# Kernel optimization log

Measured on AMD Instinct MI355X. Metric: run time of the kernel, lower is better.

The kernel has to match this reference:

```python
import jax, jax.numpy as jnp
import numpy as np

LMBDA = 100.0
GAMMA = 0.5  # resolvant_gamma


def setup_inputs() -> dict:
    key = jax.random.key(0)
    ks = jax.random.split(key, 8)
    B, Vx, Vy, C, K = 1, 5000, 5000, 128, 64
    feat_x = jax.random.normal(ks[0], (B, Vx, C), dtype=jnp.float32)
    feat_y = jax.random.normal(ks[1], (B, Vy, C), dtype=jnp.float32)
    # positive, sorted eigenvalues (Laplacian spectrum)
    evals_x = jnp.sort(jax.random.uniform(ks[2], (B, K), minval=0.01, maxval=10.0), axis=-1)
    evals_y = jnp.sort(jax.random.uniform(ks[3], (B, K), minval=0.01, maxval=10.0), axis=-1)
    # pseudo-inverse eigenvector rows, scaled ~1/sqrt(V) for realistic magnitudes
    evecs_trans_x = jax.random.normal(ks[4], (B, K, Vx), dtype=jnp.float32) / np.sqrt(Vx)
    evecs_trans_y = jax.random.normal(ks[5], (B, K, Vy), dtype=jnp.float32) / np.sqrt(Vy)
    # sqrt mass matrices: well-conditioned near-identity (must be invertible)
    eye = jnp.eye(K, dtype=jnp.float32)
    sqrtMk_x = eye[None] + 0.05 * jax.random.normal(ks[6], (B, K, K), dtype=jnp.float32)
    sqrtMk_y = eye[None] + 0.05 * jax.random.normal(ks[7], (B, K, K), dtype=jnp.float32)
    return {
        "feat_x": feat_x, "feat_y": feat_y,
        "evals_x": evals_x, "evals_y": evals_y,
        "evecs_trans_x": evecs_trans_x, "evecs_trans_y": evecs_trans_y,
        "sqrtMk_x": sqrtMk_x, "sqrtMk_y": sqrtMk_y,
    }


def _compute_fmap(fx, fy, ex, ey, Px, Py, Mx, My):
    # fx:[V,C] fy:[V,C] ex,ey:[K] Px,Py:[K,V] Mx,My:[K,K]
    A = Px @ fx                 # [K,C] spectral coeffs of source feats
    Bc = My @ (Py @ fy)         # adapt_feature=True: [K,C]
    k, m = A.shape
    vec_B = Bc.T.reshape(m * k, 1)
    # Ik = sqrtMk_y (adapt_feature, no dev_feature)
    At_Ik = jnp.kron(A.T, My)   # [m*k, k*k]
    first = At_Ik.T @ At_Ik     # [k*k, k*k]
    # adapt_mask=True branch: resolvent mask as Kronecker operators
    inv_Mx = jnp.linalg.inv(Mx)
    s = jnp.maximum(jnp.max(ex), jnp.max(ey))
    g1 = (ex / s) ** GAMMA
    g2 = (ey / s) ** GAMMA
    rn1_re = g1 / (g1 * g1 + 1.0)
    rn1_im = 1.0 / (g1 * g1 + 1.0)
    rn2_re = g2 / (g2 * g2 + 1.0)
    rn2_im = 1.0 / (g2 * g2 + 1.0)
    lx_re = jnp.kron(rn1_re[:, None] * inv_Mx, My)          # diag(rn1_re)@inv_Mx
    lx_im = jnp.kron(rn1_im[:, None] * inv_Mx, My)
    ly_re = jnp.kron(inv_Mx, My * rn2_re[None, :])          # My@diag(rn2_re)
    ly_im = jnp.kron(inv_Mx, My * rn2_im[None, :])
    D_re = ly_re - lx_re
    D_im = ly_im - lx_im
    second = D_re.T @ D_re + D_im.T @ D_im
    rhs = At_Ik.T @ vec_B
    op = first + LMBDA * second
    C = jnp.linalg.solve(op, rhs).reshape(k, k).T
    return C[None]  # [1,K,K]


def reference(feat_x, feat_y, evals_x, evals_y, evecs_trans_x, evecs_trans_y, sqrtMk_x, sqrtMk_y):
    Cxy = _compute_fmap(
        feat_x[0], feat_y[0], evals_x[0], evals_y[0],
        evecs_trans_x[0], evecs_trans_y[0], sqrtMk_x[0], sqrtMk_y[0],
    )
    return Cxy  # bidirectional=False -> Cyx is None
```

## Files before the change

kernel.cpp:

```cpp
#include <hip/hip_runtime.h>

#define NV 5000
#define LMB 100.0f
#define MAXIT 150
#define TOL 1e-10f
#define NBLK 32
#define NALL 96
#define BSZ 512

#define SV_O     0
#define CTRL_O   256
#define PART_O   2048
#define AH_O     657408
#define B0_O     665600
#define H_O      673792
#define E_O      677888
#define Z2_O     681984
#define ZH_O     686080
#define Q0_O     690176
#define LIH_O    702464
#define LIE_O    706560
#define U0_O     710656
#define LH_O     747520
#define BT_O     751616
#define RSTK_O   755712
#define LCT_O    772096
#define WG_O     788480
#define XG_O     792576
#define WS_NEED  796672

#define MS_O     PART_O
#define PRT2_O   (PART_O + 16384)
#define ZERO_N   35712

#define LCTS_S   0
#define RPK_S    12288
#define TPART_S  12800
#define TPACK_S  15920
#define SPART_S  16304
#define SM_FLOATS 21504

typedef unsigned long long u64;
union PKu { u64 u; float2 f; };

__device__ __forceinline__ float aload(const float* p) {
  return __hip_atomic_load(p, __ATOMIC_RELAXED, __HIP_MEMORY_SCOPE_AGENT);
}
__device__ __forceinline__ void astore(float* p, float v) {
  __hip_atomic_store(p, v, __ATOMIC_RELAXED, __HIP_MEMORY_SCOPE_AGENT);
}
__device__ __forceinline__ u64 aload64(const u64* p) {
  return __hip_atomic_load(p, __ATOMIC_RELAXED, __HIP_MEMORY_SCOPE_AGENT);
}
__device__ __forceinline__ void astore64(u64* p, u64 v) {
  __hip_atomic_store(p, v, __ATOMIC_RELAXED, __HIP_MEMORY_SCOPE_AGENT);
}

__device__ __forceinline__ void gbar(int* cnt, int target) {
  __syncthreads();
  if (threadIdx.x == 0) {
    __hip_atomic_fetch_add(cnt, 1, __ATOMIC_ACQ_REL, __HIP_MEMORY_SCOPE_AGENT);
    while (__hip_atomic_load(cnt, __ATOMIC_ACQUIRE, __HIP_MEMORY_SCOPE_AGENT) < target) {
      __builtin_amdgcn_s_sleep(2);
    }
  }
  __syncthreads();
}

__device__ __forceinline__ void stageN(float* dst, const float* src) {
  for (int e = threadIdx.x; e < 4096; e += BSZ)
    dst[(e >> 6) * 65 + (e & 63)] = src[e];
}
__device__ __forceinline__ void stageT(float* dst, const float* src) {
  for (int e = threadIdx.x; e < 4096; e += BSZ)
    dst[(e & 63) * 65 + (e >> 6)] = src[e];
}
__device__ __forceinline__ void mm65(const float* Ls, const float* Rs, float* D) {
  for (int e = threadIdx.x; e < 4096; e += BSZ) {
    int i = e >> 6, j = e & 63;
    float a0 = 0.f, a1 = 0.f;
#pragma unroll 8
    for (int t = 0; t < 64; t += 2) {
      a0 = fmaf(Ls[i * 65 + t], Rs[t * 65 + j], a0);
      a1 = fmaf(Ls[i * 65 + t + 1], Rs[(t + 1) * 65 + j], a1);
    }
    D[e] = a0 + a1;
  }
}
__device__ __forceinline__ void mm65L(const float* Ls, const float* Rs, float* DL) {
  for (int e = threadIdx.x; e < 4096; e += BSZ) {
    int i = e >> 6, j = e & 63;
    float a0 = 0.f, a1 = 0.f;
#pragma unroll 8
    for (int t = 0; t < 64; t += 2) {
      a0 = fmaf(Ls[i * 65 + t], Rs[t * 65 + j], a0);
      a1 = fmaf(Ls[i * 65 + t + 1], Rs[(t + 1) * 65 + j], a1);
    }
    DL[i * 65 + j] = a0 + a1;
  }
}
__device__ void mmNN_s(const float* L, const float* R, float* D, float* sm) {
  stageN(sm, L); stageN(sm + 4160, R);
  __syncthreads();
  mm65(sm, sm + 4160, D);
}

__device__ void chol_inv(const float* S, float* Li, float* Lf, float* sm) {
  float (*M)[65] = (float (*)[65])sm;
  float (*T)[65] = (float (*)[65])(sm + 64 * 65);
  int tid = threadIdx.x;
  for (int e = tid; e < 4096; e += BSZ) {
    M[e >> 6][e & 63] = S[e];
    T[e >> 6][e & 63] = 0.f;
  }
  __syncthreads();
  for (int j = 0; j < 64; ++j) {
    float pv = M[j][j];
    __syncthreads();
    float sc = rsqrtf(pv);
    if (tid < 64 - j) M[j + tid][j] *= sc;
    __syncthreads();
    int m = 63 - j, c2 = (m * (m + 1)) >> 1;
    for (int e = tid; e < c2; e += BSZ) {
      int rp = (int)((sqrtf(8.f * (float)e + 1.f) - 1.f) * 0.5f);
      while (((rp + 1) * (rp + 2)) >> 1 <= e) ++rp;
      while ((rp * (rp + 1)) >> 1 > e) --rp;
      int cp = e - ((rp * (rp + 1)) >> 1);
      int r = j + 1 + rp, c = j + 1 + cp;
      M[r][c] = fmaf(-M[r][j], M[c][j], M[r][c]);
    }
    __syncthreads();
  }
  if (tid < 64) {
    int c = tid;
    T[c][c] = 1.f / M[c][c];
    for (int r = c + 1; r < 64; ++r) {
      float s = 0.f;
      for (int t = c; t < r; ++t) s = fmaf(M[r][t], T[t][c], s);
      T[r][c] = -s / M[r][r];
    }
  }
  __syncthreads();
  if (Lf) {
    for (int e = tid; e < 4096; e += BSZ) {
      int r = e >> 6, c = e & 63;
      Lf[e] = (r >= c) ? M[r][c] : 0.f;
    }
  }
  for (int e = tid; e < 4096; e += BSZ) Li[e] = T[e >> 6][e & 63];
}

__device__ __forceinline__ float coop_apply(float* sm, const float* yv, float y_own,
                                            int lane, int wv8) {
  const float* LCTs = sm + LCTS_S;
  const float* Rpk = sm + RPK_S;
  float* Tpart = sm + TPART_S;
  float* Tpack = sm + TPACK_S;
  float* Spart = sm + SPART_S;
  float t1p[6];
#pragma unroll
  for (int p = 0; p < 6; ++p) t1p[p] = 0.f;
#pragma unroll
  for (int u = 0; u < 8; ++u) {
    int m = u * 8 + wv8;
    float yu = yv[u];
    float4 rA = *(const float4*)&Rpk[m * 8 + 0];
    float2 rB = *(const float2*)&Rpk[m * 8 + 4];
    t1p[0] = fmaf(yu, rA.x, t1p[0]);  t1p[1] = fmaf(yu, rA.y, t1p[1]);
    t1p[2] = fmaf(yu, rA.z, t1p[2]);  t1p[3] = fmaf(yu, rA.w, t1p[3]);
    t1p[4] = fmaf(yu, rB.x, t1p[4]);  t1p[5] = fmaf(yu, rB.y, t1p[5]);
  }
#pragma unroll
  for (int p = 0; p < 6; ++p) Tpart[wv8 * 390 + p * 65 + lane] = t1p[p];
  __syncthreads();
  int tid = wv8 * 64 + lane;
  if (tid < 384) {
    int tk = tid >> 1, c = tid & 1;
    int p = (tk >> 6) * 2 + c, k = tk & 63;
    Tpack[tid] = (((Tpart[0 * 390 + p * 65 + k] + Tpart[1 * 390 + p * 65 + k]) +
                   (Tpart[2 * 390 + p * 65 + k] + Tpart[3 * 390 + p * 65 + k])) +
                  ((Tpart[4 * 390 + p * 65 + k] + Tpart[5 * 390 + p * 65 + k]) +
                   (Tpart[6 * 390 + p * 65 + k] + Tpart[7 * 390 + p * 65 + k])));
  }
  __syncthreads();
  float s0 = 0.f, s1 = 0.f;
  int tk0 = wv8 * 24;
#pragma unroll 8
  for (int q = 0; q < 24; ++q) {
    int tk = tk0 + q;
    float lv = LCTs[tk * 64 + lane];
    float2 tv = *(const float2*)&Tpack[tk * 2];
    s0 = fmaf(lv, tv.x, s0);
    s1 = fmaf(lv, tv.y, s1);
  }
  Spart[wv8 * 128 + 0 * 64 + lane] = s0;
  Spart[wv8 * 128 + 1 * 64 + lane] = s1;
  __syncthreads();
  int cw = (wv8 & 1) * 64 + lane;
  return y_own + (((Spart[0 * 128 + cw] + Spart[1 * 128 + cw]) +
                   (Spart[2 * 128 + cw] + Spart[3 * 128 + cw])) +
                  ((Spart[4 * 128 + cw] + Spart[5 * 128 + cw]) +
                   (Spart[6 * 128 + cw] + Spart[7 * 128 + cw])));
}

__global__ __launch_bounds__(BSZ) void solve_kernel(const float* fx, const float* fy,
                                                    const float* ex, const float* ey,
                                                    const float* Px, const float* Py,
                                                    const float* Mx, const float* My,
                                                    float* W, float* out) {
  __shared__ float sm[SM_FLOATS] __attribute__((aligned(16)));
  __shared__ float sLd[192], sRd[192], wred[4], scal[2];
  int tid = threadIdx.x, blk = blockIdx.x;
  int* cnt = (int*)(W + CTRL_O);

  if (blk < 80) {
    int mat = (blk >= 40), seg = mat ? (blk - 40) : blk;
    const float* P = (mat ? Py : Px);
    const float* f = (mat ? fy : fx);
    int v0 = seg * 125;
    for (int e = tid; e < 8000; e += BSZ) {
      int rr = e / 125, vv = e - rr * 125;
      sm[rr * 126 + vv] = P[rr * NV + v0 + vv];
    }
    __syncthreads();
    int rg = (tid >> 5) << 2;
    int cq = (tid & 31) << 2;
    float acc[4][4];
#pragma unroll
    for (int u = 0; u < 4; ++u)
#pragma unroll
      for (int v = 0; v < 4; ++v) acc[u][v] = 0.f;
    for (int v5 = 0; v5 < 125; v5 += 5) {
      float4 fv[5];
#pragma unroll
      for (int q = 0; q < 5; ++q)
        fv[q] = *(const float4*)(f + (size_t)(v0 + v5 + q) * 128 + cq);
#pragma unroll
      for (int q = 0; q < 5; ++q) {
#pragma unroll
        for (int u = 0; u < 4; ++u) {
          float pv = sm[(rg + u) * 126 + v5 + q];
          acc[u][0] = fmaf(pv, fv[q].x, acc[u][0]);
          acc[u][1] = fmaf(pv, fv[q].y, acc[u][1]);
          acc[u][2] = fmaf(pv, fv[q].z, acc[u][2]);
          acc[u][3] = fmaf(pv, fv[q].w, acc[u][3]);
        }
      }
    }
    float* O = W + PART_O + (size_t)blk * 8192;
#pragma unroll
    for (int u = 0; u < 4; ++u) {
      float4 o = make_float4(acc[u][0], acc[u][1], acc[u][2], acc[u][3]);
      *(float4*)(O + (rg + u) * 128 + cq) = o;
    }
  } else if (blk < 82) {
    for (int e = tid; e < 4096; e += BSZ) sm[(e >> 6) * 65 + (e & 63)] = My[e];
    __syncthreads();
    int base = (blk - 80) * 2048;
    for (int e = tid; e < 2048; e += BSZ) {
      int i = (base + e) >> 6, j = (base + e) & 63;
      float a0 = 0.f, a1 = 0.f;
#pragma unroll 8
      for (int t = 0; t < 64; t += 2) {
        a0 = fmaf(sm[t * 65 + i], sm[t * 65 + j], a0);
        a1 = fmaf(sm[(t + 1) * 65 + i], sm[(t + 1) * 65 + j], a1);
      }
      W[H_O + base + e] = a0 + a1;
    }
  } else if (blk == 82) {
    if (tid < 64) {
      float vx = ex[tid], vy = ey[tid];
      float m = fmaxf(vx, vy);
#pragma unroll
      for (int o = 32; o > 0; o >>= 1) m = fmaxf(m, __shfl_xor(m, o, 64));
      float g1 = sqrtf(vx / m), g2 = sqrtf(vy / m);
      float d1 = 1.f / fmaf(g1, g1, 1.f), d2 = 1.f / fmaf(g2, g2, 1.f);
      W[SV_O + tid] = g1 * d1;
      W[SV_O + 64 + tid] = d1;
      W[SV_O + 128 + tid] = g2 * d2;
      W[SV_O + 192 + tid] = d2;
    }
  }
  gbar(cnt, NALL);
  if (blk >= NBLK) return;

  if (blk == 0) {
    chol_inv(W + H_O, W + LIH_O, W + LH_O, sm);
  } else if (blk <= 19) {
    int item = blk;
    if (item <= 8) {
      int c0 = (item - 1) * 16;
      float* ssum = sm;
      float* mxs = sm + 1088;
      for (int e = tid; e < 4096; e += BSZ) mxs[(e >> 6) * 65 + (e & 63)] = Mx[e];
      for (int e = tid; e < 1024; e += BSZ) {
        int t = e >> 4, cl = e & 15;
        float s = 0.f;
        for (int p = 0; p < 40; ++p) s += W[PART_O + (size_t)p * 8192 + t * 128 + c0 + cl];
        ssum[t * 17 + cl] = s;
      }
      __syncthreads();
      for (int e = tid; e < 1024; e += BSZ) {
        int i = e >> 4, cl = e & 15;
        float a0 = 0.f, a1 = 0.f;
#pragma unroll 8
        for (int t = 0; t < 64; t += 2) {
          a0 = fmaf(mxs[t * 65 + i], ssum[t * 17 + cl], a0);
          a1 = fmaf(mxs[(t + 1) * 65 + i], ssum[(t + 1) * 17 + cl], a1);
        }
        W[AH_O + i * 128 + c0 + cl] = a0 + a1;
      }
    } else if (item <= 16) {
      int base = (item - 9) * 1024;
      for (int e = tid; e < 1024; e += BSZ) {
        float s = 0.f;
        for (int p = 0; p < 40; ++p) s += W[PART_O + (size_t)(40 + p) * 8192 + base + e];
        W[B0_O + base + e] = s;
      }
    } else {
      if (tid < 256) sm[tid] = W[SV_O + tid];
      __syncthreads();
      int t = item - 17;
      for (int e = tid; e < 4096; e += BSZ) {
        int k = e >> 6, b = e & 63;
        float h = W[H_O + e], v;
        if (t == 0) v = h * (sm[128 + k] * sm[128 + b] + sm[192 + k] * sm[192 + b]);
        else if (t == 1) v = h * (sm[128 + k] + sm[128 + b]);
        else v = h * (sm[192 + k] + sm[192 + b]);
        W[Q0_O + t * 4096 + e] = v;
      }
    }
  }
  gbar(cnt, NALL + NBLK);

  if (blk < 4) {
    for (int e = tid; e < 8192; e += BSZ) {
      int i = e >> 7, c = e & 127;
      sm[c * 65 + i] = W[AH_O + e];
    }
    __syncthreads();
    int i0 = blk * 16;
    for (int e = tid; e < 1024; e += BSZ) {
      int i = i0 + (e >> 6), j = e & 63;
      float a0 = 0.f, a1 = 0.f;
#pragma unroll 8
      for (int c = 0; c < 128; c += 2) {
        a0 = fmaf(sm[c * 65 + i], sm[c * 65 + j], a0);
        a1 = fmaf(sm[(c + 1) * 65 + i], sm[(c + 1) * 65 + j], a1);
      }
      float acc = a0 + a1;
      if (i == j) {
        float a = W[SV_O + i], b = W[SV_O + 64 + i];
        acc += LMB * (a * a + b * b);
      }
      W[E_O + i * 64 + j] = acc;
    }
  } else if (blk < 8) {
    int i0 = (blk - 4) * 16;
    for (int e = tid; e < 8192; e += BSZ) {
      int j = e >> 7, c = e & 127;
      sm[c * 65 + j] = W[B0_O + e];
    }
    for (int e = tid; e < 2048; e += BSZ) {
      int il = e >> 7, c = e & 127;
      sm[8320 + c * 17 + il] = W[AH_O + (i0 + il) * 128 + c];
    }
    __syncthreads();
    for (int e = tid; e < 1024; e += BSZ) {
      int il = e >> 6, j = e & 63;
      float a0 = 0.f, a1 = 0.f;
#pragma unroll 8
      for (int c = 0; c < 128; c += 2) {
        a0 = fmaf(sm[8320 + c * 17 + il], sm[c * 65 + j], a0);
        a1 = fmaf(sm[8320 + (c + 1) * 17 + il], sm[(c + 1) * 65 + j], a1);
      }
      W[Z2_O + (i0 + il) * 64 + j] = a0 + a1;
    }
  } else if (blk < 11) {
    int t = blk - 8;
    mmNN_s(W + LIH_O, W + Q0_O + t * 4096, W + U0_O + t * 4096, sm);
  } else {
    for (int e = (blk - 11) * BSZ + tid; e < ZERO_N; e += 21 * BSZ)
      W[MS_O + e] = 0.f;
  }
  gbar(cnt, NALL + 2 * NBLK);

  if (blk == 0) chol_inv(W + E_O, W + LIE_O, nullptr, sm);
  else if (blk == 1) mmNN_s(W + Z2_O, W + LH_O, W + ZH_O, sm);
  else if (blk < 5) {
    int t = blk - 2;
    stageN(sm, W + U0_O + t * 4096);
    stageT(sm + 4160, W + LIH_O);
    __syncthreads();
    mm65L(sm, sm + 4160, sm + 8320);
    __syncthreads();
    for (int e = tid; e < 4096; e += BSZ) {
      int a = e >> 6, b = e & 63;
      W[RSTK_O + t * 4096 + e] = 0.5f * (sm[8320 + a * 65 + b] + sm[8320 + b * 65 + a]);
    }
  }
  gbar(cnt, NALL + 3 * NBLK);

  if (blk == 0) mmNN_s(W + LIE_O, W + ZH_O, W + BT_O, sm);
  else if (blk == 1) {
    stageN(sm, W + LIE_O);
    stageT(sm + 4160, W + LIE_O);
    __syncthreads();
    mm65L(sm, sm + 4160, sm + 8320);
    __syncthreads();
    for (int e = tid; e < 4096; e += BSZ) {
      int k = e >> 6, i = e & 63;
      W[LCT_O + e] = LMB * 0.5f * (sm[8320 + k * 65 + i] + sm[8320 + i * 65 + k]);
    }
  } else if (blk < 4) {
    float* dv = sLd;
    if (tid < 64) dv[tid] = W[SV_O + ((blk == 2) ? tid : 64 + tid)];
    stageN(sm, W + LIE_O);
    __syncthreads();
    for (int e = tid; e < 4096; e += BSZ) {
      int jq = e >> 6, k = e & 63;
      sm[4160 + k * 65 + jq] = sm[jq * 65 + k] * dv[k];
    }
    __syncthreads();
    mm65L(sm, sm + 4160, sm + 8320);
    __syncthreads();
    int t = blk - 1;
    for (int e = tid; e < 4096; e += BSZ) {
      int k = e >> 6, i = e & 63;
      W[LCT_O + t * 4096 + e] = -LMB * 0.5f * (sm[8320 + k * 65 + i] + sm[8320 + i * 65 + k]);
    }
  }
  gbar(cnt, NALL + 4 * NBLK);

  int lane = tid & 63, wv8 = tid >> 6;
  int jown = blk * 2 + wv8;
  const float* BTp = W + BT_O;
  const float* LCTp = W + LCT_O;
  const float* RSTKp = W + RSTK_O;
  u64* MS = (u64*)(W + MS_O);
  u64* PR2 = (u64*)(W + PRT2_O);

  for (int e = tid; e < 12288; e += BSZ) sm[LCTS_S + e] = LCTp[e];
  if (tid < 384) {
    int m = tid / 6, p = tid - m * 6;
    int t = p >> 1, c = p & 1;
    sm[RPK_S + m * 8 + p] = RSTKp[(t * 64 + blk * 2 + c) * 64 + m];
  }
  if (tid < 192) {
    int t = tid >> 6, i = tid & 63;
    sLd[tid] = LCTp[t * 4096 + i * 64 + i];
    sRd[tid] = RSTKp[t * 4096 + i * 64 + i];
  }
  __syncthreads();
  float yv0[8];
#pragma unroll
  for (int u = 0; u < 8; ++u) {
    int col = u * 8 + wv8;
    float den = 1.f + sLd[lane] * sRd[col] + sLd[64 + lane] * sRd[64 + col] +
                sLd[128 + lane] * sRd[128 + col];
    yv0[u] = BTp[lane * 64 + col] / den;
  }
  float invd = 0.f, u_l = 0.f, r_l = 0.f, m_l = 0.f;
  if (wv8 < 2) {
    invd = 1.f / (1.f + sLd[lane] * sRd[jown] + sLd[64 + lane] * sRd[64 + jown] +
                  sLd[128 + lane] * sRd[128 + jown]);
    u_l = BTp[lane * 64 + jown] * invd;
    r_l = BTp[lane * 64 + jown];
  }
  float w_l = coop_apply(sm, yv0, u_l, lane, wv8);
  if (wv8 < 2) {
    m_l = invd * w_l;
    PKu pk; pk.f = make_float2(m_l, 1.f);
    astore64(MS + jown * 64 + lane, pk.u);
    float vr = r_l * u_l, vw = w_l * u_l;
#pragma unroll
    for (int o = 32; o; o >>= 1) { vr += __shfl_down(vr, o, 64); vw += __shfl_down(vw, o, 64); }
    if (lane == 0) { wred[wv8 * 2] = vr; wred[wv8 * 2 + 1] = vw; }
  }
  __syncthreads();
  if (tid == 0) {
    PKu a, b;
    a.f = make_float2(wred[0] + wred[2], 1.f);
    b.f = make_float2(wred[1] + wred[3], 1.f);
    astore64(PR2 + (size_t)blk * 2, a.u);
    astore64(PR2 + (size_t)blk * 2 + 1, b.u);
  }

  float p_l = 0.f, q_l = 0.f, z_l = 0.f, s_l = 0.f, x_l = 0.f;
  float gprev = 1.f, aprev = 1.f, g0b = 1.f;
  int sl = lane & 31;
  for (int j = 0; j < MAXIT; ++j) {
    unsigned sbits = __float_as_uint((float)(j + 1));
    const u64* msrc = MS + (size_t)(j & 1) * 4096;
    u64 raw[8];
#pragma unroll
    for (int u = 0; u < 8; ++u) raw[u] = aload64(msrc + u * BSZ + tid);
    const u64* ps = PR2 + ((size_t)j * 32 + sl) * 2;
    u64 ra = 0, rb = 0;
    if (wv8 == 0) { ra = aload64(ps); rb = aload64(ps + 1); }
    {
      int spins = 0;
      for (;;) {
        bool ok = true;
#pragma unroll
        for (int u = 0; u < 8; ++u) ok = ok && ((unsigned)(raw[u] >> 32) == sbits);
        if (__all(ok)) break;
        if (++spins > 64) {
          __hip_atomic_load(msrc + tid, __ATOMIC_ACQUIRE, __HIP_MEMORY_SCOPE_AGENT);
          spins = 0;
        }
#pragma unroll
        for (int u = 0; u < 8; ++u)
          if ((unsigned)(raw[u] >> 32) != sbits) raw[u] = aload64(msrc + u * BSZ + tid);
      }
    }
    float mv[8];
#pragma unroll
    for (int u = 0; u < 8; ++u) mv[u] = __uint_as_float((unsigned)raw[u]);
    float n_l = coop_apply(sm, mv, m_l, lane, wv8);
    if (wv8 == 0) {
      int spins = 0;
      for (;;) {
        bool ok = ((unsigned)(ra >> 32) == sbits) && ((unsigned)(rb >> 32) == sbits);
        if (__all(ok)) break;
        if (++spins > 64) {
          __hip_atomic_load(ps, __ATOMIC_ACQUIRE, __HIP_MEMORY_SCOPE_AGENT);
          spins = 0;
        }
        if ((unsigned)(ra >> 32) != sbits) ra = aload64(ps);
        if ((unsigned)(rb >> 32) != sbits) rb = aload64(ps + 1);
      }
      float pr = __uint_as_float((unsigned)ra), pw = __uint_as_float((unsigned)rb);
#pragma unroll
      for (int mm = 1; mm < 32; mm <<= 1) {
        pr += __shfl_xor(pr, mm, 64);
        pw += __shfl_xor(pw, mm, 64);
      }
      if (lane == 0) { scal[0] = pr; scal[1] = pw; }
    }
    __syncthreads();
    float gjb = scal[0], djb = scal[1];
    if (j == 0) g0b = gjb;
    if (j > 0 && fabsf(gjb) < TOL * fabsf(g0b)) break;
    if (wv8 < 2) {
      float bj = (j == 0) ? 0.f : gjb / gprev;
      float aj = (j == 0) ? gjb / djb : gjb / (djb - bj * gjb / aprev);
      float z_n = fmaf(bj, z_l, n_l);
      float w_n = fmaf(-aj, z_n, w_l);
      float m_n = invd * w_n;
      PKu pk; pk.f = make_float2(m_n, (float)(j + 2));
      astore64(MS + (size_t)((j + 1) & 1) * 4096 + jown * 64 + lane, pk.u);
      q_l = fmaf(bj, q_l, m_l);
      s_l = fmaf(bj, s_l, w_l);
      p_l = fmaf(bj, p_l, u_l);
      x_l = fmaf(aj, p_l, x_l);
      r_l = fmaf(-aj, s_l, r_l);
      u_l = fmaf(-aj, q_l, u_l);
      z_l = z_n; w_l = w_n; m_l = m_n;
      float vr = r_l * u_l, vw = w_l * u_l;
#pragma unroll
      for (int o = 32; o; o >>= 1) { vr += __shfl_down(vr, o, 64); vw += __shfl_down(vw, o, 64); }
      if (lane == 0) { wred[wv8 * 2] = vr; wred[wv8 * 2 + 1] = vw; }
      gprev = gjb; aprev = aj;
    }
    __syncthreads();
    if (tid == 0) {
      PKu a, b;
      a.f = make_float2(wred[0] + wred[2], (float)(j + 2));
      b.f = make_float2(wred[1] + wred[3], (float)(j + 2));
      astore64(PR2 + ((size_t)(j + 1) * 32 + blk) * 2, a.u);
      astore64(PR2 + ((size_t)(j + 1) * 32 + blk) * 2 + 1, b.u);
    }
  }
  if (wv8 < 2) astore(W + XG_O + jown * 64 + lane, x_l);
  gbar(cnt, NALL + 5 * NBLK);

  if (blk == 0) {
    float* Ys = sm;
    float* Ms2 = sm + 4160;
    for (int e = tid; e < 4096; e += BSZ) Ys[(e >> 6) * 65 + (e & 63)] = aload(W + XG_O + e);
    for (int e = tid; e < 4096; e += BSZ) Ms2[(e >> 6) * 65 + (e & 63)] = W[LIE_O + e];
    __syncthreads();
    for (int e = tid; e < 4096; e += BSZ) {
      int t = e >> 6, b = e & 63;
      float acc = 0.f;
#pragma unroll 8
      for (int a = 0; a < 64; ++a) acc = fmaf(Ms2[a * 65 + t], Ys[b * 65 + a], acc);
      W[WG_O + t * 64 + b] = acc;
    }
    __syncthreads();
    for (int e = tid; e < 4096; e += BSZ) Ys[(e >> 6) * 65 + (e & 63)] = W[WG_O + e];
    for (int e = tid; e < 4096; e += BSZ) Ms2[(e >> 6) * 65 + (e & 63)] = W[LIH_O + e];
    __syncthreads();
    for (int e = tid; e < 4096; e += BSZ) {
      int t = e >> 6, c = e & 63;
      float acc = 0.f;
#pragma unroll 8
      for (int b = 0; b < 64; ++b) acc = fmaf(Ys[t * 65 + b], Ms2[b * 65 + c], acc);
      W[WG_O + t * 64 + c] = acc;
    }
    __syncthreads();
    for (int e = tid; e < 4096; e += BSZ) Ys[(e >> 6) * 65 + (e & 63)] = W[WG_O + e];
    for (int e = tid; e < 4096; e += BSZ) Ms2[(e & 63) * 65 + (e >> 6)] = Mx[e];
    __syncthreads();
    for (int e = tid; e < 4096; e += BSZ) {
      int r = e >> 6, c = e & 63;
      float acc = 0.f;
#pragma unroll 8
      for (int t = 0; t < 64; ++t) acc = fmaf(Ms2[t * 65 + c], Ys[t * 65 + r], acc);
      out[e] = acc;
    }
  }
}

extern "C" void kernel_launch(void* const* d_in, const int* in_sizes, int n_in,
                              void* d_out, int out_size, void* d_ws, size_t ws_size,
                              hipStream_t stream) {
  const float* fx = (const float*)d_in[0];
  const float* fy = (const float*)d_in[1];
  const float* ex = (const float*)d_in[2];
  const float* ey = (const float*)d_in[3];
  const float* Px = (const float*)d_in[4];
  const float* Py = (const float*)d_in[5];
  const float* Mx = (const float*)d_in[6];
  const float* My = (const float*)d_in[7];
  float* out = (float*)d_out;
  float* W = (float*)d_ws;

  if (ws_size < (size_t)WS_NEED * sizeof(float)) {
    hipMemsetAsync(d_out, 0, (size_t)out_size * sizeof(float), stream);
    return;
  }

  hipMemsetAsync(W + CTRL_O, 0, 256, stream);
  solve_kernel<<<NALL, BSZ, 0, stream>>>(fx, fy, ex, ey, Px, Py, Mx, My, W, out);
}
```

Baseline: 342.4 us.

## Shard grid barrier counters and overlap dependency waits with partial matvec

```diff
diff --git a/kernel.cpp b/kernel.cpp
--- a/kernel.cpp
+++ b/kernel.cpp
@@ -56,11 +56,18 @@
   __hip_atomic_store(p, v, __ATOMIC_RELAXED, __HIP_MEMORY_SCOPE_AGENT);
 }
 
-__device__ __forceinline__ void gbar(int* cnt, int target) {
-  __syncthreads();
-  if (threadIdx.x == 0) {
-    __hip_atomic_fetch_add(cnt, 1, __ATOMIC_ACQ_REL, __HIP_MEMORY_SCOPE_AGENT);
-    while (__hip_atomic_load(cnt, __ATOMIC_ACQUIRE, __HIP_MEMORY_SCOPE_AGENT) < target) {
+__device__ __forceinline__ void gbar(int* cb, int phase, int blk, int per) {
+  __syncthreads();
+  if (threadIdx.x == 0)
+    __hip_atomic_fetch_add(cb + phase * 128 + (blk & 7) * 16, 1,
+                           __ATOMIC_ACQ_REL, __HIP_MEMORY_SCOPE_AGENT);
+  if (threadIdx.x < 64) {
+    for (;;) {
+      int v = (threadIdx.x < 8)
+        ? __hip_atomic_load(cb + phase * 128 + threadIdx.x * 16,
+                            __ATOMIC_ACQUIRE, __HIP_MEMORY_SCOPE_AGENT)
+        : per;
+      if (__all(v >= per)) break;
       __builtin_amdgcn_s_sleep(2);
     }
   }
@@ -115,10 +122,7 @@
   }
   __syncthreads();
   for (int j = 0; j < 64; ++j) {
-    float pv = M[j][j];
-    __syncthreads();
-    float sc = rsqrtf(pv);
-    if (tid < 64 - j) M[j + tid][j] *= sc;
+    if (tid < 63 - j) M[j + 1 + tid][j] *= rsqrtf(M[j][j]);
     __syncthreads();
     int m = 63 - j, c2 = (m * (m + 1)) >> 1;
     for (int e = tid; e < c2; e += BSZ) {
@@ -133,18 +137,18 @@
   }
   if (tid < 64) {
     int c = tid;
-    T[c][c] = 1.f / M[c][c];
+    T[c][c] = rsqrtf(M[c][c]);
     for (int r = c + 1; r < 64; ++r) {
       float s = 0.f;
       for (int t = c; t < r; ++t) s = fmaf(M[r][t], T[t][c], s);
-      T[r][c] = -s / M[r][r];
+      T[r][c] = -s * rsqrtf(M[r][r]);
     }
   }
   __syncthreads();
   if (Lf) {
     for (int e = tid; e < 4096; e += BSZ) {
       int r = e >> 6, c = e & 63;
-      Lf[e] = (r >= c) ? M[r][c] : 0.f;
+      Lf[e] = (r > c) ? M[r][c] : ((r == c) ? sqrtf(M[r][c]) : 0.f);
     }
   }
   for (int e = tid; e < 4096; e += BSZ) Li[e] = T[e >> 6][e & 63];
@@ -211,7 +215,7 @@
   __shared__ float sm[SM_FLOATS] __attribute__((aligned(16)));
   __shared__ float sLd[192], sRd[192], wred[4], scal[2];
   int tid = threadIdx.x, blk = blockIdx.x;
-  int* cnt = (int*)(W + CTRL_O);
+  int* cb = (int*)(W + CTRL_O);
 
   if (blk < 80) {
     int mat = (blk >= 40), seg = mat ? (blk - 40) : blk;
@@ -281,7 +285,7 @@
       W[SV_O + 192 + tid] = d2;
     }
   }
-  gbar(cnt, NALL);
+  gbar(cb, 0, blk, 12);
   if (blk >= NBLK) return;
 
   if (blk == 0) {
@@ -331,7 +335,7 @@
       }
     }
   }
-  gbar(cnt, NALL + NBLK);
+  gbar(cb, 1, blk, 4);
 
   if (blk < 4) {
     for (int e = tid; e < 8192; e += BSZ) {
@@ -383,7 +387,7 @@
     for (int e = (blk - 11) * BSZ + tid; e < ZERO_N; e += 21 * BSZ)
       W[MS_O + e] = 0.f;
   }
-  gbar(cnt, NALL + 2 * NBLK);
+  gbar(cb, 2, blk, 4);
 
   if (blk == 0) chol_inv(W + E_O, W + LIE_O, nullptr, sm);
   else if (blk == 1) mmNN_s(W + Z2_O, W + LH_O, W + ZH_O, sm);
@@ -399,7 +403,7 @@
       W[RSTK_O + t * 4096 + e] = 0.5f * (sm[8320 + a * 65 + b] + sm[8320 + b * 65 + a]);
     }
   }
-  gbar(cnt, NALL + 3 * NBLK);
+  gbar(cb, 3, blk, 4);
 
   if (blk == 0) mmNN_s(W + LIE_O, W + ZH_O, W + BT_O, sm);
   else if (blk == 1) {
@@ -430,7 +434,7 @@
       W[LCT_O + t * 4096 + e] = -LMB * 0.5f * (sm[8320 + k * 65 + i] + sm[8320 + i * 65 + k]);
     }
   }
-  gbar(cnt, NALL + 4 * NBLK);
+  gbar(cb, 4, blk, 4);
 
   int lane = tid & 63, wv8 = tid >> 6;
   int jown = blk * 2 + wv8;
@@ -439,6 +443,11 @@
   const float* RSTKp = W + RSTK_O;
   u64* MS = (u64*)(W + MS_O);
   u64* PR2 = (u64*)(W + PRT2_O);
+  const float* LCTs = sm + LCTS_S;
+  const float* Rpk = sm + RPK_S;
+  float* Tpart = sm + TPART_S;
+  float* Tpack = sm + TPACK_S;
+  float* Spart = sm + SPART_S;
 
   for (int e = tid; e < 12288; e += BSZ) sm[LCTS_S + e] = LCTp[e];
   if (tid < 384) {
@@ -492,40 +501,63 @@
   for (int j = 0; j < MAXIT; ++j) {
     unsigned sbits = __float_as_uint((float)(j + 1));
     const u64* msrc = MS + (size_t)(j & 1) * 4096;
-    u64 raw[8];
-#pragma unroll
-    for (int u = 0; u < 8; ++u) raw[u] = aload64(msrc + u * BSZ + tid);
     const u64* ps = PR2 + ((size_t)j * 32 + sl) * 2;
     u64 ra = 0, rb = 0;
     if (wv8 == 0) { ra = aload64(ps); rb = aload64(ps + 1); }
-    {
-      int spins = 0;
-      for (;;) {
-        bool ok = true;
-#pragma unroll
-        for (int u = 0; u < 8; ++u) ok = ok && ((unsigned)(raw[u] >> 32) == sbits);
-        if (__all(ok)) break;
-        if (++spins > 64) {
-          __hip_atomic_load(msrc + tid, __ATOMIC_ACQUIRE, __HIP_MEMORY_SCOPE_AGENT);
-          spins = 0;
+    float t1p[6];
+#pragma unroll
+    for (int p = 0; p < 6; ++p) t1p[p] = 0.f;
+    u64 raw8[8];
+#pragma unroll
+    for (int u = 0; u < 8; ++u) raw8[u] = aload64(msrc + u * BSZ + tid);
+    unsigned done = 0;
+    int spins = 0;
+    while (done != 0xFFu) {
+#pragma unroll
+      for (int u = 0; u < 8; ++u) {
+        if (!((done >> u) & 1u)) {
+          u64 v = raw8[u];
+          if ((unsigned)(v >> 32) == sbits) {
+            float yu = __uint_as_float((unsigned)v);
+            int m = u * 8 + wv8;
+            float4 rA = *(const float4*)&Rpk[m * 8 + 0];
+            float2 rB = *(const float2*)&Rpk[m * 8 + 4];
+            t1p[0] = fmaf(yu, rA.x, t1p[0]);
+            t1p[1] = fmaf(yu, rA.y, t1p[1]);
+            t1p[2] = fmaf(yu, rA.z, t1p[2]);
+            t1p[3] = fmaf(yu, rA.w, t1p[3]);
+            t1p[4] = fmaf(yu, rB.x, t1p[4]);
+            t1p[5] = fmaf(yu, rB.y, t1p[5]);
+            done |= (1u << u);
+          } else {
+            raw8[u] = aload64(msrc + u * BSZ + tid);
+          }
         }
-#pragma unroll
-        for (int u = 0; u < 8; ++u)
-          if ((unsigned)(raw[u] >> 32) != sbits) raw[u] = aload64(msrc + u * BSZ + tid);
-      }
-    }
-    float mv[8];
-#pragma unroll
-    for (int u = 0; u < 8; ++u) mv[u] = __uint_as_float((unsigned)raw[u]);
-    float n_l = coop_apply(sm, mv, m_l, lane, wv8);
-    if (wv8 == 0) {
-      int spins = 0;
+      }
+      if (done != 0xFFu && ++spins > 64) {
+        __hip_atomic_load(msrc + tid, __ATOMIC_ACQUIRE, __HIP_MEMORY_SCOPE_AGENT);
+        spins = 0;
+      }
+    }
+#pragma unroll
+    for (int p = 0; p < 6; ++p) Tpart[wv8 * 390 + p * 65 + lane] = t1p[p];
+    __syncthreads();
+    if (wv8 >= 2) {
+      int z = tid - 128;
+      int tk = z >> 1, c = z & 1;
+      int p = (tk >> 6) * 2 + c, k = tk & 63;
+      Tpack[z] = (((Tpart[0 * 390 + p * 65 + k] + Tpart[1 * 390 + p * 65 + k]) +
+                   (Tpart[2 * 390 + p * 65 + k] + Tpart[3 * 390 + p * 65 + k])) +
+                  ((Tpart[4 * 390 + p * 65 + k] + Tpart[5 * 390 + p * 65 + k]) +
+                   (Tpart[6 * 390 + p * 65 + k] + Tpart[7 * 390 + p * 65 + k])));
+    } else if (wv8 == 0) {
+      int spins2 = 0;
       for (;;) {
         bool ok = ((unsigned)(ra >> 32) == sbits) && ((unsigned)(rb >> 32) == sbits);
         if (__all(ok)) break;
-        if (++spins > 64) {
+        if (++spins2 > 64) {
           __hip_atomic_load(ps, __ATOMIC_ACQUIRE, __HIP_MEMORY_SCOPE_AGENT);
-          spins = 0;
+          spins2 = 0;
         }
         if ((unsigned)(ra >> 32) != sbits) ra = aload64(ps);
         if ((unsigned)(rb >> 32) != sbits) rb = aload64(ps + 1);
@@ -542,7 +574,25 @@
     float gjb = scal[0], djb = scal[1];
     if (j == 0) g0b = gjb;
     if (j > 0 && fabsf(gjb) < TOL * fabsf(g0b)) break;
+    float s0 = 0.f, s1 = 0.f;
+    int tk0 = wv8 * 24;
+#pragma unroll 8
+    for (int q = 0; q < 24; ++q) {
+      int tk = tk0 + q;
+      float lv = LCTs[tk * 64 + lane];
+      float2 tv = *(const float2*)&Tpack[tk * 2];
+      s0 = fmaf(lv, tv.x, s0);
+      s1 = fmaf(lv, tv.y, s1);
+    }
+    Spart[wv8 * 128 + 0 * 64 + lane] = s0;
+    Spart[wv8 * 128 + 1 * 64 + lane] = s1;
+    __syncthreads();
     if (wv8 < 2) {
+      int cw = wv8 * 64 + lane;
+      float n_l = m_l + (((Spart[0 * 128 + cw] + Spart[1 * 128 + cw]) +
+                          (Spart[2 * 128 + cw] + Spart[3 * 128 + cw])) +
+                         ((Spart[4 * 128 + cw] + Spart[5 * 128 + cw]) +
+                          (Spart[6 * 128 + cw] + Spart[7 * 128 + cw])));
       float bj = (j == 0) ? 0.f : gjb / gprev;
       float aj = (j == 0) ? gjb / djb : gjb / (djb - bj * gjb / aprev);
       float z_n = fmaf(bj, z_l, n_l);
@@ -573,7 +623,7 @@
     }
   }
   if (wv8 < 2) astore(W + XG_O + jown * 64 + lane, x_l);
-  gbar(cnt, NALL + 5 * NBLK);
+  gbar(cb, 5, blk, 4);
 
   if (blk == 0) {
     float* Ys = sm;
@@ -632,6 +682,6 @@
     return;
   }
 
-  hipMemsetAsync(W + CTRL_O, 0, 256, stream);
+  hipMemsetAsync(W + CTRL_O, 0, 3072, stream);
   solve_kernel<<<NALL, BSZ, 0, stream>>>(fx, fy, ex, ey, Px, Py, Mx, My, W, out);
 }
```

Result: slower. 351.6 us (+2.7%).

## Replace Jacobi preconditioner with block-Jacobi Cholesky inverse and add stagnation exit

Applied to the files above, without the earlier changes.

```diff
diff --git a/kernel.cpp b/kernel.cpp
--- a/kernel.cpp
+++ b/kernel.cpp
@@ -4,6 +4,7 @@
 #define LMB 100.0f
 #define MAXIT 150
 #define TOL 1e-10f
+#define PATIENCE 30
 #define NBLK 32
 #define NALL 96
 #define BSZ 512
@@ -38,7 +39,9 @@
 #define TPART_S  12800
 #define TPACK_S  15920
 #define SPART_S  16304
-#define SM_FLOATS 21504
+#define SCRA_S   12800
+#define SCRB_S   21120
+#define SM_FLOATS 29440
 
 typedef unsigned long long u64;
 union PKu { u64 u; float2 f; };
@@ -203,13 +206,26 @@
                    (Spart[6 * 128 + cw] + Spart[7 * 128 + cw])));
 }
 
+#define BJ_MATVEC(OUTV, INV)                                               \
+  {                                                                        \
+    wbuf[wv8 * 64 + lane] = (INV);                                         \
+    float mac0 = 0.f, mac1 = 0.f;                                          \
+    _Pragma("unroll")                                                      \
+    for (int kq = 0; kq < 16; ++kq) {                                      \
+      float4 wv4 = *(const float4*)&wbuf[wv8 * 64 + kq * 4];               \
+      mac0 = fmaf(bc[kq].x, wv4.x, fmaf(bc[kq].y, wv4.y, mac0));           \
+      mac1 = fmaf(bc[kq].z, wv4.z, fmaf(bc[kq].w, wv4.w, mac1));           \
+    }                                                                      \
+    (OUTV) = mac0 + mac1;                                                  \
+  }
+
 __global__ __launch_bounds__(BSZ) void solve_kernel(const float* fx, const float* fy,
                                                     const float* ex, const float* ey,
                                                     const float* Px, const float* Py,
                                                     const float* Mx, const float* My,
                                                     float* W, float* out) {
   __shared__ float sm[SM_FLOATS] __attribute__((aligned(16)));
-  __shared__ float sLd[192], sRd[192], wred[4], scal[2];
+  __shared__ float sLd[192], sRd[192], wred[4], scal[2], wbuf[128];
   int tid = threadIdx.x, blk = blockIdx.x;
   int* cnt = (int*)(W + CTRL_O);
 
@@ -433,12 +449,13 @@
   gbar(cnt, NALL + 4 * NBLK);
 
   int lane = tid & 63, wv8 = tid >> 6;
-  int jown = blk * 2 + wv8;
+  int jown = blk * 2 + (wv8 & 1);
   const float* BTp = W + BT_O;
   const float* LCTp = W + LCT_O;
   const float* RSTKp = W + RSTK_O;
   u64* MS = (u64*)(W + MS_O);
   u64* PR2 = (u64*)(W + PRT2_O);
+  const float* LCTs = sm + LCTS_S;
 
   for (int e = tid; e < 12288; e += BSZ) sm[LCTS_S + e] = LCTp[e];
   if (tid < 384) {
@@ -448,28 +465,122 @@
   }
   if (tid < 192) {
     int t = tid >> 6, i = tid & 63;
-    sLd[tid] = LCTp[t * 4096 + i * 64 + i];
     sRd[tid] = RSTKp[t * 4096 + i * 64 + i];
   }
   __syncthreads();
-  float yv0[8];
-#pragma unroll
-  for (int u = 0; u < 8; ++u) {
-    int col = u * 8 + wv8;
-    float den = 1.f + sLd[lane] * sRd[col] + sLd[64 + lane] * sRd[64 + col] +
-                sLd[128 + lane] * sRd[128 + col];
-    yv0[u] = BTp[lane * 64 + col] / den;
-  }
-  float invd = 0.f, u_l = 0.f, r_l = 0.f, m_l = 0.f;
+
+  {
+    float* M0 = sm + SCRA_S;
+    float* T0 = sm + SCRA_S + 4160;
+    float* M1 = sm + SCRB_S;
+    float* T1 = sm + SCRB_S + 4160;
+    int jc0 = blk * 2, jc1 = blk * 2 + 1;
+    float r00 = sRd[jc0], r01 = sRd[64 + jc0], r02 = sRd[128 + jc0];
+    float r10 = sRd[jc1], r11 = sRd[64 + jc1], r12 = sRd[128 + jc1];
+    for (int e = tid; e < 4096; e += BSZ) {
+      int r = e >> 6, c = e & 63;
+      float a = LCTs[r * 64 + c];
+      float b2 = LCTs[4096 + r * 64 + c];
+      float c3 = LCTs[8192 + r * 64 + c];
+      float dg = (r == c) ? 1.f : 0.f;
+      M0[r * 65 + c] = dg + r00 * a + r01 * b2 + r02 * c3;
+      M1[r * 65 + c] = dg + r10 * a + r11 * b2 + r12 * c3;
+      T0[r * 65 + c] = 0.f;
+      T1[r * 65 + c] = 0.f;
+    }
+    __syncthreads();
+    for (int jj = 0; jj < 64; ++jj) {
+      if (tid < 63 - jj) {
+        M0[(jj + 1 + tid) * 65 + jj] *= rsqrtf(M0[jj * 65 + jj]);
+      } else if (tid >= 256 && tid - 256 < 63 - jj) {
+        int t2 = tid - 256;
+        M1[(jj + 1 + t2) * 65 + jj] *= rsqrtf(M1[jj * 65 + jj]);
+      }
+      __syncthreads();
+      int m = 63 - jj, c2 = (m * (m + 1)) >> 1;
+      for (int e = tid; e < 2 * c2; e += BSZ) {
+        int wh = (e >= c2);
+        int ee = e - wh * c2;
+        float* MM = wh ? M1 : M0;
+        int rp = (int)((sqrtf(8.f * (float)ee + 1.f) - 1.f) * 0.5f);
+        while (((rp + 1) * (rp + 2)) >> 1 <= ee) ++rp;
+        while ((rp * (rp + 1)) >> 1 > ee) --rp;
+        int cp = ee - ((rp * (rp + 1)) >> 1);
+        int r = jj + 1 + rp, c = jj + 1 + cp;
+        MM[r * 65 + c] = fmaf(-MM[r * 65 + jj], MM[c * 65 + jj], MM[r * 65 + c]);
+      }
+      __syncthreads();
+    }
+    if (tid < 128) {
+      int wh = tid >> 6, c = tid & 63;
+      float* MM = wh ? M1 : M0;
+      float* TT = wh ? T1 : T0;
+      TT[c * 65 + c] = rsqrtf(MM[c * 65 + c]);
+      for (int r = c + 1; r < 64; ++r) {
+        float s = 0.f;
+        for (int t = c; t < r; ++t) s = fmaf(MM[r * 65 + t], TT[t * 65 + c], s);
+        TT[r * 65 + c] = -s * rsqrtf(MM[r * 65 + r]);
+      }
+    }
+    __syncthreads();
+    for (int e = tid; e < 8192; e += BSZ) {
+      int wh = e >> 12, ee = e & 4095;
+      int r = ee >> 6, l = ee & 63;
+      const float* TT = wh ? T1 : T0;
+      float acc0 = 0.f, acc1 = 0.f;
+      int k0 = (r > l) ? r : l;
+      for (int k = k0; k < 64; k += 2) {
+        acc0 = fmaf(TT[k * 65 + r], TT[k * 65 + l], acc0);
+        if (k + 1 < 64) acc1 = fmaf(TT[(k + 1) * 65 + r], TT[(k + 1) * 65 + l], acc1);
+      }
+      float* DP = wh ? M1 : M0;
+      DP[(l >> 2) * 260 + r * 4 + (l & 3)] = acc0 + acc1;
+    }
+    __syncthreads();
+  }
+  float4 bc[16];
   if (wv8 < 2) {
-    invd = 1.f / (1.f + sLd[lane] * sRd[jown] + sLd[64 + lane] * sRd[64 + jown] +
-                  sLd[128 + lane] * sRd[128 + jown]);
-    u_l = BTp[lane * 64 + jown] * invd;
+    const float* BP = sm + (wv8 ? SCRB_S : SCRA_S);
+#pragma unroll
+    for (int kq = 0; kq < 16; ++kq)
+      bc[kq] = *(const float4*)&BP[kq * 260 + lane * 4];
+  }
+  __syncthreads();
+
+  float u_l = 0.f, r_l = 0.f, m_l = 0.f, w_l = 0.f;
+  if (wv8 < 2) {
     r_l = BTp[lane * 64 + jown];
-  }
-  float w_l = coop_apply(sm, yv0, u_l, lane, wv8);
+    BJ_MATVEC(u_l, r_l);
+    PKu pk; pk.f = make_float2(u_l, 1.f);
+    astore64(MS + 4096 + jown * 64 + lane, pk.u);
+  }
+  {
+    unsigned sbits = __float_as_uint(1.0f);
+    const u64* msrc = MS + 4096;
+    u64 raw[8];
+#pragma unroll
+    for (int u = 0; u < 8; ++u) raw[u] = aload64(msrc + u * BSZ + tid);
+    int spins = 0;
+    for (;;) {
+      bool ok = true;
+#pragma unroll
+      for (int u = 0; u < 8; ++u) ok = ok && ((unsigned)(raw[u] >> 32) == sbits);
+      if (__all(ok)) break;
+      if (++spins > 64) {
+        __hip_atomic_load(msrc + tid, __ATOMIC_ACQUIRE, __HIP_MEMORY_SCOPE_AGENT);
+        spins = 0;
+      }
+#pragma unroll
+      for (int u = 0; u < 8; ++u)
+        if ((unsigned)(raw[u] >> 32) != sbits) raw[u] = aload64(msrc + u * BSZ + tid);
+    }
+    float mv[8];
+#pragma unroll
+    for (int u = 0; u < 8; ++u) mv[u] = __uint_as_float((unsigned)raw[u]);
+    w_l = coop_apply(sm, mv, u_l, lane, wv8);
+  }
   if (wv8 < 2) {
-    m_l = invd * w_l;
+    BJ_MATVEC(m_l, w_l);
     PKu pk; pk.f = make_float2(m_l, 1.f);
     astore64(MS + jown * 64 + lane, pk.u);
     float vr = r_l * u_l, vw = w_l * u_l;
@@ -488,6 +599,8 @@
 
   float p_l = 0.f, q_l = 0.f, z_l = 0.f, s_l = 0.f, x_l = 0.f;
   float gprev = 1.f, aprev = 1.f, g0b = 1.f;
+  float gmin = 3.4e38f;
+  int lastimp = 0;
   int sl = lane & 31;
   for (int j = 0; j < MAXIT; ++j) {
     unsigned sbits = __float_as_uint((float)(j + 1));
@@ -541,13 +654,16 @@
     __syncthreads();
     float gjb = scal[0], djb = scal[1];
     if (j == 0) g0b = gjb;
-    if (j > 0 && fabsf(gjb) < TOL * fabsf(g0b)) break;
+    float agj = fabsf(gjb);
+    if (agj < 0.9f * gmin) { gmin = agj; lastimp = j; }
+    if (j > 0 && (agj < TOL * fabsf(g0b) || (j - lastimp) > PATIENCE)) break;
     if (wv8 < 2) {
       float bj = (j == 0) ? 0.f : gjb / gprev;
       float aj = (j == 0) ? gjb / djb : gjb / (djb - bj * gjb / aprev);
       float z_n = fmaf(bj, z_l, n_l);
       float w_n = fmaf(-aj, z_n, w_l);
-      float m_n = invd * w_n;
+      float m_n;
+      BJ_MATVEC(m_n, w_n);
       PKu pk; pk.f = make_float2(m_n, (float)(j + 2));
       astore64(MS + (size_t)((j + 1) & 1) * 4096 + jown * 64 + lane, pk.u);
       q_l = fmaf(bj, q_l, m_l);
```

Result: slower. 491.2 us (+43.5%).
